# Kernel optimization log

Measured on AMD Instinct MI355X. Metric: run time of the kernel, lower is better.

## Reference

```python
import jax, jax.numpy as jnp
import numpy as np

MOS = 100        # max_output_size
IOU_T = 0.9      # iou_threshold
SCORE_T = 0.9    # score_threshold (sigma=0 -> hard NMS; also subsumes the 0.5 decode threshold)
PRE_NMS = 2048   # top-k candidates kept before greedy NMS (fixed-shape jit-friendly form)


def setup_inputs() -> dict:
    key = jax.random.key(0)
    k1, k2 = jax.random.split(key)
    B, H, W, K = 32, 192, 192, 9
    score_map = jax.random.uniform(k1, (B, H, W, K), dtype=jnp.float32)
    delta_map = jax.random.normal(k2, (B, H, W, 4 * K), dtype=jnp.float32) * 0.1
    # realistic normalized grid anchors: 3 scales x 3 aspect ratios, format (xmin, xmax, ymin, ymax)
    scales = jnp.array([0.05, 0.1, 0.2], jnp.float32)
    ratios = jnp.array([0.5, 1.0, 2.0], jnp.float32)
    ws = (scales[:, None] * jnp.sqrt(ratios)[None, :]).reshape(-1)  # [K]
    hs = (scales[:, None] / jnp.sqrt(ratios)[None, :]).reshape(-1)  # [K]
    cx = ((jnp.arange(W, dtype=jnp.float32) + 0.5) / W)[None, :, None]  # [1,W,1]
    cy = ((jnp.arange(H, dtype=jnp.float32) + 0.5) / H)[:, None, None]  # [H,1,1]
    xmin, xmax, ymin, ymax = jnp.broadcast_arrays(cx - ws / 2, cx + ws / 2, cy - hs / 2, cy + hs / 2)
    anchors = jnp.stack([xmin, xmax, ymin, ymax], axis=-1).astype(jnp.float32)  # [H,W,K,4]
    return {"score_map": score_map, "delta_map": delta_map, "anchors": anchors}


def _decode(anchors, deltas):
    # anchors: [H,W,K,4] (xmin,xmax,ymin,ymax); deltas: [B,H,W,K,4] (tx,ty,tw,th)
    xa = (anchors[..., 0] + anchors[..., 1]) * 0.5
    ya = (anchors[..., 2] + anchors[..., 3]) * 0.5
    wa = anchors[..., 1] - anchors[..., 0]
    ha = anchors[..., 3] - anchors[..., 2]
    tx, ty, tw, th = deltas[..., 0], deltas[..., 1], deltas[..., 2], deltas[..., 3]
    x = tx * wa + xa
    y = ty * ha + ya
    w = jnp.exp(tw) * wa
    h = jnp.exp(th) * ha
    # one-sided clips exactly as in the original
    xmin = jnp.maximum(x - w * 0.5, 0.0)
    xmax = jnp.minimum(x + w * 0.5, 1.0)
    ymin = jnp.maximum(y - h * 0.5, 0.0)
    ymax = jnp.minimum(y + h * 0.5, 1.0)
    # original reorders boxes for tf NMS as (ymax, xmin, ymin, xmax) and returns them in that order
    return jnp.stack([ymax, xmin, ymin, xmax], axis=-1)


def _iou_one_vs_all(box, boxes):
    # box layout: (ymax, xmin, ymin, xmax)
    y2a, x1a, y1a, x2a = box[0], box[1], box[2], box[3]
    y2b, x1b, y1b, x2b = boxes[:, 0], boxes[:, 1], boxes[:, 2], boxes[:, 3]
    area_a = jnp.maximum(y2a - y1a, 0.0) * jnp.maximum(x2a - x1a, 0.0)
    area_b = jnp.maximum(y2b - y1b, 0.0) * jnp.maximum(x2b - x1b, 0.0)
    ih = jnp.maximum(jnp.minimum(y2a, y2b) - jnp.maximum(y1a, y1b), 0.0)
    iw = jnp.maximum(jnp.minimum(x2a, x2b) - jnp.maximum(x1a, x1b), 0.0)
    inter = ih * iw
    return inter / (area_a + area_b - inter + 1e-9)


def _nms_one(scores, boxes):
    # scores: [N], boxes: [N,4]. Hard greedy NMS over top PRE_NMS candidates above SCORE_T.
    masked = jnp.where(scores > SCORE_T, scores, -jnp.inf)
    top_s, top_i = jax.lax.top_k(masked, PRE_NMS)
    top_b = boxes[top_i]  # [PRE_NMS, 4]

    def step(s, _):
        idx = jnp.argmax(s)
        valid = s[idx] > SCORE_T
        box = top_b[idx]
        iou = _iou_one_vs_all(box, top_b)
        s = jnp.where(iou > IOU_T, -jnp.inf, s).at[idx].set(-jnp.inf)
        return s, jnp.where(valid, box, jnp.zeros_like(box))

    _, out = jax.lax.scan(step, top_s, None, length=MOS)
    return out  # [MOS, 4], zero-padded past the last kept box


def reference(score_map, delta_map, anchors):
    B = score_map.shape[0]
    H, W, K = anchors.shape[:3]
    deltas = delta_map.reshape(B, H, W, K, 4)
    boxes = _decode(anchors, deltas).reshape(B, H * W * K, 4)
    scores = score_map.reshape(B, H * W * K)
    return jax.vmap(_nms_one)(scores, boxes)  # [B, MOS, 4]
```

## Files before the change

kernel.cpp:

```cpp
#include <hip/hip_runtime.h>
#include <stdint.h>

#pragma clang fp contract(off)

typedef unsigned long long u64;
typedef unsigned int u32;

#define NH 192
#define NW 192
#define NK 9
#define NPB (NH * NW * NK)
#define PRE_NMS 2048
#define CAP 4096
#define FAST_CAP 512
#define FAST_K 256
#define MOS 100
#define SCORE_T_BITS 0x3F666666u
#define SPEC_BITS   0x3F7E0000u
#define ONE_BITS 0x3F800000u
#define IOU_T 0.9f


__global__ void zero_meta(int* __restrict__ meta, int n) {
    int i = blockIdx.x * blockDim.x + threadIdx.x;
    if (i < n) meta[i] = 0;
}

__global__ void spec_compact_kernel(const uint4* __restrict__ scores,
                                    int* __restrict__ hist,
                                    int* __restrict__ cnt,
                                    u64* __restrict__ keys) {
    __shared__ u64 stage[4096];
    __shared__ int lh[256];
    __shared__ int lcount, lbase;
    const int t = threadIdx.x;
    lh[t] = 0;
    if (t == 0) lcount = 0;
    __syncthreads();
    const int b = blockIdx.y;
    const int base_i = blockIdx.x * 4096;
    const uint4* sp = scores + (size_t)b * (NPB / 4) + (size_t)blockIdx.x * 1024;
#pragma unroll
    for (int i = 0; i < 4; ++i) {
        uint4 v = sp[t + i * 256];
        int ei = base_i + (t + i * 256) * 4;
        u32 uu[4] = {v.x, v.y, v.z, v.w};
#pragma unroll
        for (int c = 0; c < 4; ++c) {
            u32 u = uu[c];
            if (u > SCORE_T_BITS) {
                atomicAdd(&lh[(u >> 16) & 0xFF], 1);
                if (u >= SPEC_BITS) {
                    int p = atomicAdd(&lcount, 1);
                    u32 idx = (u32)(ei + c);
                    stage[p] = ((u64)u << 32) | (u64)(~idx);
                }
            }
        }
    }
    __syncthreads();
    if (t == 0) lbase = atomicAdd(&cnt[b], lcount);
    if (lh[t] != 0) atomicAdd(&hist[b * 256 + t], lh[t]);
    __syncthreads();
    const int nb = lcount, gb = lbase;
    u64* kb = keys + (size_t)b * CAP;
    for (int i = t; i < nb; i += 256) {
        int gp = gb + i;
        if (gp < CAP) kb[gp] = stage[i];
    }
}

__global__ void fixup_kernel(const int* __restrict__ hist, int* __restrict__ cnt,
                             u32* __restrict__ bound, int* __restrict__ flag, int B) {
    int b = blockIdx.x * blockDim.x + threadIdx.x;
    if (b >= B) return;
    int c = cnt[b];
    if (c >= PRE_NMS && c <= CAP) { bound[b] = SPEC_BITS; flag[b] = 0; return; }
    int cum = 0, tv = 0;
    for (int v = 255; v >= 0; --v) {
        cum += hist[b * 256 + v];
        if (cum >= PRE_NMS) { tv = v; break; }
    }
    u32 bd = ((u32)(0x3F00 + tv)) << 16;
    if (bd < SCORE_T_BITS + 1) bd = SCORE_T_BITS + 1;
    bound[b] = bd; flag[b] = 1; cnt[b] = 0;
}

__global__ void repair_compact_kernel(const uint4* __restrict__ scores,
                                      const u32* __restrict__ bound,
                                      const int* __restrict__ flag,
                                      int* __restrict__ cnt,
                                      u64* __restrict__ keys) {
    const int b = blockIdx.y;
    if (!flag[b]) return;
    __shared__ u64 stage[4096];
    __shared__ int lcount, lbase;
    const int t = threadIdx.x;
    if (t == 0) lcount = 0;
    __syncthreads();
    const u32 bd = bound[b];
    const int base_i = blockIdx.x * 4096;
    const uint4* sp = scores + (size_t)b * (NPB / 4) + (size_t)blockIdx.x * 1024;
#pragma unroll
    for (int i = 0; i < 4; ++i) {
        uint4 v = sp[t + i * 256];
        int ei = base_i + (t + i * 256) * 4;
        u32 uu[4] = {v.x, v.y, v.z, v.w};
#pragma unroll
        for (int c = 0; c < 4; ++c) {
            if (uu[c] >= bd) {
                int p = atomicAdd(&lcount, 1);
                u32 idx = (u32)(ei + c);
                stage[p] = ((u64)uu[c] << 32) | (u64)(~idx);
            }
        }
    }
    __syncthreads();
    if (t == 0) lbase = atomicAdd(&cnt[b], lcount);
    __syncthreads();
    const int nb = lcount, gb = lbase;
    u64* kb = keys + (size_t)b * CAP;
    for (int i = t; i < nb; i += 256) {
        int gp = gb + i;
        if (gp < CAP) kb[gp] = stage[i];
    }
}

__device__ __forceinline__ float4 decode_box(u64 key, int b,
                                             const float4* __restrict__ anchors4,
                                             const float4* __restrict__ deltas4) {
    u32 idx = ~(u32)(key & 0xFFFFFFFFu);
    float4 a = anchors4[idx];
    float4 d = deltas4[(size_t)b * NPB + idx];
    float xa = (a.x + a.y) * 0.5f;
    float ya = (a.z + a.w) * 0.5f;
    float wa = a.y - a.x;
    float ha = a.w - a.z;
    float x = d.x * wa + xa;
    float y = d.y * ha + ya;
    float w = expf(d.z) * wa;
    float h = expf(d.w) * ha;
    float4 bx;
    bx.x = fminf(y + h * 0.5f, 1.f);
    bx.y = fmaxf(x - w * 0.5f, 0.f);
    bx.z = fmaxf(y - h * 0.5f, 0.f);
    bx.w = fminf(x + w * 0.5f, 1.f);
    return bx;
}

__device__ __forceinline__ int wave_nms(const float4* __restrict__ boxes, int n,
                                        float4* __restrict__ out4, int lane) {
    float4 pb0 = make_float4(0.f, 0.f, 0.f, 0.f), pb1 = pb0;
    float pa0 = 0.f, pa1 = 0.f;
    int np = 0;
#define ACCEPT(cb, ar) do { \
        if (lane == (np & 63)) { \
            if (np < 64) { pb0 = cb; pa0 = ar; } else { pb1 = cb; pa1 = ar; } \
            out4[np] = cb; } \
        ++np; } while (0)
    for (int j = 0; j < n; j += 2) {
        const bool have1 = (j + 1 < n);
        float4 c0 = boxes[j];
        float4 c1 = boxes[have1 ? j + 1 : j];
        float ar0 = fmaxf(c0.x - c0.z, 0.f) * fmaxf(c0.w - c0.y, 0.f);
        float ar1 = fmaxf(c1.x - c1.z, 0.f) * fmaxf(c1.w - c1.y, 0.f);
        bool s0 = false, s1 = false;
        if (lane < np) {
            float ih = fmaxf(fminf(pb0.x, c0.x) - fmaxf(pb0.z, c0.z), 0.f);
            float iw = fmaxf(fminf(pb0.w, c0.w) - fmaxf(pb0.y, c0.y), 0.f);
            float inter = ih * iw;
            s0 = inter / (pa0 + ar0 - inter + 1e-9f) > IOU_T;
            ih = fmaxf(fminf(pb0.x, c1.x) - fmaxf(pb0.z, c1.z), 0.f);
            iw = fmaxf(fminf(pb0.w, c1.w) - fmaxf(pb0.y, c1.y), 0.f);
            inter = ih * iw;
            s1 = inter / (pa0 + ar1 - inter + 1e-9f) > IOU_T;
        }
        if (lane + 64 < np) {
            float ih = fmaxf(fminf(pb1.x, c0.x) - fmaxf(pb1.z, c0.z), 0.f);
            float iw = fmaxf(fminf(pb1.w, c0.w) - fmaxf(pb1.y, c0.y), 0.f);
            float inter = ih * iw;
            s0 = s0 || (inter / (pa1 + ar0 - inter + 1e-9f) > IOU_T);
            ih = fmaxf(fminf(pb1.x, c1.x) - fmaxf(pb1.z, c1.z), 0.f);
            iw = fmaxf(fminf(pb1.w, c1.w) - fmaxf(pb1.y, c1.y), 0.f);
            inter = ih * iw;
            s1 = s1 || (inter / (pa1 + ar1 - inter + 1e-9f) > IOU_T);
        }
        bool acc0 = !__any(s0);
        bool acc1 = !__any(s1);
        if (acc0) {
            ACCEPT(c0, ar0);
            if (np == MOS) break;
            if (have1 && acc1) {
                float ih = fmaxf(fminf(c0.x, c1.x) - fmaxf(c0.z, c1.z), 0.f);
                float iw = fmaxf(fminf(c0.w, c1.w) - fmaxf(c0.y, c1.y), 0.f);
                float inter = ih * iw;
                if (!(inter / (ar0 + ar1 - inter + 1e-9f) > IOU_T)) {
                    ACCEPT(c1, ar1);
                    if (np == MOS) break;
                }
            }
        } else if (have1 && acc1) {
            ACCEPT(c1, ar1);
            if (np == MOS) break;
        }
    }
#undef ACCEPT
    return np;
}

__global__ __launch_bounds__(256) void sort_nms_kernel(
        const float* __restrict__ deltas, const float* __restrict__ anchors,
        const int* __restrict__ cnt, const u32* __restrict__ bound,
        const u64* __restrict__ keys, float* __restrict__ out) {
    __shared__ __align__(16) u64 key_s[CAP];
    __shared__ __align__(16) float4 boxes[PRE_NMS];
    __shared__ u64 fast_k[FAST_CAP];
    __shared__ int lh[256];
    __shared__ int s_cnt, s_nsel, s_flag, s_cbin, s_sh;

    const int t = threadIdx.x;
    const int b = blockIdx.x;
    const int nc = min(cnt[b], CAP);
    const u64* kb = keys + (size_t)b * CAP;
    const float4* anchors4 = (const float4*)anchors;
    const float4* deltas4  = (const float4*)deltas;
    float4* out4 = (float4*)out + (size_t)b * MOS;

    lh[t] = 0;
    if (t == 0) {
        s_cnt = 0;
        u32 dmax = ONE_BITS - bound[b];
        int bits = 32 - __builtin_clz(dmax);
        s_sh = (bits > 8) ? (bits - 8) : 0;
    }
    __syncthreads();
    const int sh = s_sh;

#pragma unroll
    for (int p = 0; p < CAP / 256; ++p) {
        int i = t + p * 256;
        u64 k = (i < nc) ? kb[i] : 0ULL;
        key_s[i] = k;
        if (i < nc) {
            u32 d = ONE_BITS - (u32)(k >> 32);
            u32 bin = d >> sh;
            if (bin > 255u) bin = 255u;
            atomicAdd(&lh[bin], 1);
        }
    }
    for (int i = t; i < FAST_CAP; i += 256) fast_k[i] = 0ULL;
    __syncthreads();

    if (t == 0) {
        int cum = 0; bool hit = false;
        for (int v = 0; v < 256; ++v) {
            cum += lh[v];
            if (cum >= FAST_K) {
                if (cum > FAST_CAP) { s_nsel = cum - lh[v]; s_cbin = v - 1; }
                else                { s_nsel = cum;         s_cbin = v; }
                hit = true; break;
            }
        }
        if (!hit) { s_nsel = cum; s_cbin = 255; }
    }
    __syncthreads();
    const int cbin = s_cbin;
    const int n_sel = s_nsel;

#pragma unroll
    for (int p = 0; p < CAP / 256; ++p) {
        int i = t + p * 256;
        if (i < nc) {
            u64 k = key_s[i];
            u32 d = ONE_BITS - (u32)(k >> 32);
            u32 bin = d >> sh;
            if (bin > 255u) bin = 255u;
            if ((int)bin <= cbin) fast_k[atomicAdd(&s_cnt, 1)] = k;
        }
    }
    __syncthreads();

    for (int k = 2; k <= FAST_CAP; k <<= 1) {
        for (int j = k >> 1; j > 0; j >>= 1) {
            for (int i = t; i < FAST_CAP; i += 256) {
                int ix = i ^ j;
                if (ix > i) {
                    u64 a = fast_k[i], c = fast_k[ix];
                    bool up = ((i & k) == 0);
                    if (up ? (a < c) : (a > c)) { fast_k[i] = c; fast_k[ix] = a; }
                }
            }
            __syncthreads();
        }
    }

    for (int i = t; i < FAST_CAP; i += 256)
        boxes[i] = (i < n_sel) ? decode_box(fast_k[i], b, anchors4, deltas4)
                               : make_float4(0.f, 0.f, 0.f, 0.f);
    __syncthreads();

    if (t < 64) {
        int np = wave_nms(boxes, n_sel, out4, t);
        bool success = (np == MOS) || (n_sel == nc);
        if (success)
            for (int i = np + t; i < MOS; i += 64)
                out4[i] = make_float4(0.f, 0.f, 0.f, 0.f);
        if (t == 0) s_flag = success ? 1 : 0;
    }
    __syncthreads();
    if (s_flag) return;

    for (int k = 2; k <= CAP; k <<= 1) {
        for (int j = k >> 1; j > 0; j >>= 1) {
            for (int i = t; i < CAP; i += 256) {
                int ix = i ^ j;
                if (ix > i) {
                    u64 a = key_s[i], c = key_s[ix];
                    bool up = ((i & k) == 0);
                    if (up ? (a < c) : (a > c)) { key_s[i] = c; key_s[ix] = a; }
                }
            }
            __syncthreads();
        }
    }
    const int nvalid = min(nc, PRE_NMS);
    for (int i = t; i < PRE_NMS; i += 256)
        boxes[i] = (i < nvalid) ? decode_box(key_s[i], b, anchors4, deltas4)
                                : make_float4(0.f, 0.f, 0.f, 0.f);
    __syncthreads();
    if (t < 64) {
        int np = wave_nms(boxes, nvalid, out4, t);
        for (int i = np + t; i < MOS; i += 64)
            out4[i] = make_float4(0.f, 0.f, 0.f, 0.f);
    }
}

extern "C" void kernel_launch(void* const* d_in, const int* in_sizes, int n_in,
                              void* d_out, int out_size, void* d_ws, size_t ws_size,
                              hipStream_t stream) {
    const float* score_map = (const float*)d_in[0];
    const float* delta_map = (const float*)d_in[1];
    const float* anchors   = (const float*)d_in[2];
    float* out = (float*)d_out;
    const int B = in_sizes[0] / NPB;

    char* ws = (char*)d_ws;
    size_t off = 0;
    int* hist  = (int*)(ws + off); off += (size_t)B * 256 * 4;
    int* cnt   = (int*)(ws + off); off += (size_t)B * 4;
    u32* bound = (u32*)(ws + off); off += (size_t)B * 4;
    int* flag  = (int*)(ws + off); off += (size_t)B * 4;
    u64* keys  = (u64*)(ws + off);

    const int meta_n = B * 256 + B;
    zero_meta<<<(meta_n + 255) / 256, 256, 0, stream>>>(hist, meta_n);
    spec_compact_kernel<<<dim3(NPB / 4096, B), 256, 0, stream>>>(
        (const uint4*)score_map, hist, cnt, keys);
    fixup_kernel<<<1, 64, 0, stream>>>(hist, cnt, bound, flag, B);
    repair_compact_kernel<<<dim3(NPB / 4096, B), 256, 0, stream>>>(
        (const uint4*)score_map, bound, flag, cnt, keys);
    sort_nms_kernel<<<B, 256, 0, stream>>>(delta_map, anchors, cnt, bound, keys, out);
}
```

Baseline: 301.0 us.

## Drop histogram and repair launches, move fallback selection into sort kernel

The speculative compaction kernel no longer builds a per-batch histogram and uses a smaller staging buffer. The separate fixup and repair kernels are removed. A batch whose speculative count falls outside the valid range now rescans its scores inside the sort/NMS block, using a two-level histogram to pick a finer bound. The NMS loop also prefetches the next pair of candidate boxes from shared memory. This cuts two kernel launches and the histogram atomics on the common path, but the rare fallback path becomes a serial per-block scan of a whole image.

```diff
diff --git a/kernel.cpp b/kernel.cpp
--- a/kernel.cpp
+++ b/kernel.cpp
@@ -21,20 +21,17 @@
 #define IOU_T 0.9f
 
 
-__global__ void zero_meta(int* __restrict__ meta, int n) {
-    int i = blockIdx.x * blockDim.x + threadIdx.x;
-    if (i < n) meta[i] = 0;
+__global__ void zero_cnt(int* __restrict__ cnt, int n) {
+    int i = threadIdx.x;
+    if (i < n) cnt[i] = 0;
 }
 
 __global__ void spec_compact_kernel(const uint4* __restrict__ scores,
-                                    int* __restrict__ hist,
                                     int* __restrict__ cnt,
                                     u64* __restrict__ keys) {
-    __shared__ u64 stage[4096];
-    __shared__ int lh[256];
+    __shared__ u64 stage[512];
     __shared__ int lcount, lbase;
     const int t = threadIdx.x;
-    lh[t] = 0;
     if (t == 0) lcount = 0;
     __syncthreads();
     const int b = blockIdx.y;
@@ -48,77 +45,17 @@
 #pragma unroll
         for (int c = 0; c < 4; ++c) {
             u32 u = uu[c];
-            if (u > SCORE_T_BITS) {
-                atomicAdd(&lh[(u >> 16) & 0xFF], 1);
-                if (u >= SPEC_BITS) {
-                    int p = atomicAdd(&lcount, 1);
-                    u32 idx = (u32)(ei + c);
-                    stage[p] = ((u64)u << 32) | (u64)(~idx);
-                }
-            }
-        }
-    }
-    __syncthreads();
-    if (t == 0) lbase = atomicAdd(&cnt[b], lcount);
-    if (lh[t] != 0) atomicAdd(&hist[b * 256 + t], lh[t]);
-    __syncthreads();
-    const int nb = lcount, gb = lbase;
-    u64* kb = keys + (size_t)b * CAP;
-    for (int i = t; i < nb; i += 256) {
-        int gp = gb + i;
-        if (gp < CAP) kb[gp] = stage[i];
-    }
-}
-
-__global__ void fixup_kernel(const int* __restrict__ hist, int* __restrict__ cnt,
-                             u32* __restrict__ bound, int* __restrict__ flag, int B) {
-    int b = blockIdx.x * blockDim.x + threadIdx.x;
-    if (b >= B) return;
-    int c = cnt[b];
-    if (c >= PRE_NMS && c <= CAP) { bound[b] = SPEC_BITS; flag[b] = 0; return; }
-    int cum = 0, tv = 0;
-    for (int v = 255; v >= 0; --v) {
-        cum += hist[b * 256 + v];
-        if (cum >= PRE_NMS) { tv = v; break; }
-    }
-    u32 bd = ((u32)(0x3F00 + tv)) << 16;
-    if (bd < SCORE_T_BITS + 1) bd = SCORE_T_BITS + 1;
-    bound[b] = bd; flag[b] = 1; cnt[b] = 0;
-}
-
-__global__ void repair_compact_kernel(const uint4* __restrict__ scores,
-                                      const u32* __restrict__ bound,
-                                      const int* __restrict__ flag,
-                                      int* __restrict__ cnt,
-                                      u64* __restrict__ keys) {
-    const int b = blockIdx.y;
-    if (!flag[b]) return;
-    __shared__ u64 stage[4096];
-    __shared__ int lcount, lbase;
-    const int t = threadIdx.x;
-    if (t == 0) lcount = 0;
-    __syncthreads();
-    const u32 bd = bound[b];
-    const int base_i = blockIdx.x * 4096;
-    const uint4* sp = scores + (size_t)b * (NPB / 4) + (size_t)blockIdx.x * 1024;
-#pragma unroll
-    for (int i = 0; i < 4; ++i) {
-        uint4 v = sp[t + i * 256];
-        int ei = base_i + (t + i * 256) * 4;
-        u32 uu[4] = {v.x, v.y, v.z, v.w};
-#pragma unroll
-        for (int c = 0; c < 4; ++c) {
-            if (uu[c] >= bd) {
+            if (u >= SPEC_BITS) {
                 int p = atomicAdd(&lcount, 1);
                 u32 idx = (u32)(ei + c);
-                stage[p] = ((u64)uu[c] << 32) | (u64)(~idx);
+                if (p < 512) stage[p] = ((u64)u << 32) | (u64)(~idx);
             }
         }
     }
     __syncthreads();
     if (t == 0) lbase = atomicAdd(&cnt[b], lcount);
     __syncthreads();
-    const int nb = lcount, gb = lbase;
+    const int nb = min(lcount, 512), gb = lbase;
     u64* kb = keys + (size_t)b * CAP;
     for (int i = t; i < nb; i += 256) {
         int gp = gb + i;
@@ -153,15 +90,21 @@
     float4 pb0 = make_float4(0.f, 0.f, 0.f, 0.f), pb1 = pb0;
     float pa0 = 0.f, pa1 = 0.f;
     int np = 0;
+    if (n <= 0) return 0;
 #define ACCEPT(cb, ar) do { \
         if (lane == (np & 63)) { \
             if (np < 64) { pb0 = cb; pa0 = ar; } else { pb1 = cb; pa1 = ar; } \
             out4[np] = cb; } \
         ++np; } while (0)
+    float4 n0 = boxes[0];
+    float4 n1 = boxes[(1 < n) ? 1 : 0];
     for (int j = 0; j < n; j += 2) {
         const bool have1 = (j + 1 < n);
-        float4 c0 = boxes[j];
-        float4 c1 = boxes[have1 ? j + 1 : j];
+        float4 c0 = n0, c1 = n1;
+        int jn0 = (j + 2 < n) ? j + 2 : j;
+        int jn1 = (j + 3 < n) ? j + 3 : jn0;
+        n0 = boxes[jn0];
+        n1 = boxes[jn1];
         float ar0 = fmaxf(c0.x - c0.z, 0.f) * fmaxf(c0.w - c0.y, 0.f);
         float ar1 = fmaxf(c1.x - c1.z, 0.f) * fmaxf(c1.w - c1.y, 0.f);
         bool s0 = false, s1 = false;
@@ -209,40 +152,128 @@
 }
 
 __global__ __launch_bounds__(256) void sort_nms_kernel(
+        const uint4* __restrict__ scores,
         const float* __restrict__ deltas, const float* __restrict__ anchors,
-        const int* __restrict__ cnt, const u32* __restrict__ bound,
-        const u64* __restrict__ keys, float* __restrict__ out) {
+        const int* __restrict__ cnt, const u64* __restrict__ keys,
+        float* __restrict__ out) {
     __shared__ __align__(16) u64 key_s[CAP];
     __shared__ __align__(16) float4 boxes[PRE_NMS];
     __shared__ u64 fast_k[FAST_CAP];
     __shared__ int lh[256];
-    __shared__ int s_cnt, s_nsel, s_flag, s_cbin, s_sh;
+    __shared__ int s_cnt, s_nsel, s_flag, s_cbin, s_sh, s_nc;
+    __shared__ u32 s_bd;
+    __shared__ int s_tv, s_cumabove, s_skipB;
 
     const int t = threadIdx.x;
     const int b = blockIdx.x;
-    const int nc = min(cnt[b], CAP);
-    const u64* kb = keys + (size_t)b * CAP;
     const float4* anchors4 = (const float4*)anchors;
     const float4* deltas4  = (const float4*)deltas;
     float4* out4 = (float4*)out + (size_t)b * MOS;
 
-    lh[t] = 0;
+    const int nc0 = cnt[b];
+    const bool valid = (nc0 >= PRE_NMS && nc0 <= CAP);
+
+    if (valid) {
+        const u64* kb = keys + (size_t)b * CAP;
+#pragma unroll
+        for (int p = 0; p < CAP / 256; ++p) {
+            int i = t + p * 256;
+            key_s[i] = (i < nc0) ? kb[i] : 0ULL;
+        }
+        if (t == 0) { s_nc = nc0; s_bd = SPEC_BITS; }
+        __syncthreads();
+    } else {
+        const uint4* sp = scores + (size_t)b * (NPB / 4);
+        lh[t] = 0;
+        __syncthreads();
+        for (int i = t; i < NPB / 4; i += 256) {
+            uint4 v = sp[i];
+            u32 uu[4] = {v.x, v.y, v.z, v.w};
+#pragma unroll
+            for (int c = 0; c < 4; ++c)
+                if (uu[c] > SCORE_T_BITS) atomicAdd(&lh[(uu[c] >> 16) & 0xFF], 1);
+        }
+        __syncthreads();
+        if (t == 0) {
+            int cum = 0, tv = -1, cumab = 0;
+            for (int v = 255; v >= 0; --v) {
+                int h = lh[v];
+                if (cum + h >= PRE_NMS) { tv = v; cumab = cum; break; }
+                cum += h;
+            }
+            if (tv < 0) { s_bd = SCORE_T_BITS + 1; s_skipB = 1; }
+            else        { s_tv = tv; s_cumabove = cumab; s_skipB = 0; }
+        }
+        __syncthreads();
+        if (!s_skipB) {
+            const int tv = s_tv;
+            lh[t] = 0;
+            __syncthreads();
+            for (int i = t; i < NPB / 4; i += 256) {
+                uint4 v = sp[i];
+                u32 uu[4] = {v.x, v.y, v.z, v.w};
+#pragma unroll
+                for (int c = 0; c < 4; ++c)
+                    if (uu[c] > SCORE_T_BITS && (int)((uu[c] >> 16) & 0xFF) == tv)
+                        atomicAdd(&lh[(uu[c] >> 8) & 0xFF], 1);
+            }
+            __syncthreads();
+            if (t == 0) {
+                int cum = s_cumabove, iv = 0;
+                for (int v = 255; v >= 0; --v) {
+                    cum += lh[v];
+                    if (cum >= PRE_NMS) {
+                        iv = (cum > CAP && v < 255) ? v + 1 : v;
+                        break;
+                    }
+                }
+                u32 bd = (((u32)(0x3F00 + tv)) << 16) | ((u32)iv << 8);
+                if (bd < SCORE_T_BITS + 1) bd = SCORE_T_BITS + 1;
+                s_bd = bd;
+            }
+        }
+        __syncthreads();
+        if (t == 0) s_cnt = 0;
+        __syncthreads();
+        const u32 bd = s_bd;
+        for (int i = t; i < NPB / 4; i += 256) {
+            uint4 v = sp[i];
+            u32 uu[4] = {v.x, v.y, v.z, v.w};
+#pragma unroll
+            for (int c = 0; c < 4; ++c) {
+                if (uu[c] >= bd) {
+                    int p = atomicAdd(&s_cnt, 1);
+                    u32 idx = (u32)(i * 4 + c);
+                    if (p < CAP) key_s[p] = ((u64)uu[c] << 32) | (u64)(~idx);
+                }
+            }
+        }
+        __syncthreads();
+        if (t == 0) s_nc = min(s_cnt, CAP);
+        __syncthreads();
+        for (int p = 0; p < CAP / 256; ++p) {
+            int i = t + p * 256;
+            if (i >= s_nc) key_s[i] = 0ULL;
+        }
+        __syncthreads();
+    }
+
+    const int nc = s_nc;
     if (t == 0) {
         s_cnt = 0;
-        u32 dmax = ONE_BITS - bound[b];
+        u32 dmax = ONE_BITS - s_bd;
         int bits = 32 - __builtin_clz(dmax);
         s_sh = (bits > 8) ? (bits - 8) : 0;
     }
+    lh[t] = 0;
     __syncthreads();
     const int sh = s_sh;
 
 #pragma unroll
     for (int p = 0; p < CAP / 256; ++p) {
         int i = t + p * 256;
-        u64 k = (i < nc) ? kb[i] : 0ULL;
-        key_s[i] = k;
         if (i < nc) {
-            u32 d = ONE_BITS - (u32)(k >> 32);
+            u32 d = ONE_BITS - (u32)(key_s[i] >> 32);
             u32 bin = d >> sh;
             if (bin > 255u) bin = 255u;
             atomicAdd(&lh[bin], 1);
@@ -345,19 +376,13 @@
     const int B = in_sizes[0] / NPB;
 
     char* ws = (char*)d_ws;
-    size_t off = 0;
-    int* hist  = (int*)(ws + off); off += (size_t)B * 256 * 4;
-    int* cnt   = (int*)(ws + off); off += (size_t)B * 4;
-    u32* bound = (u32*)(ws + off); off += (size_t)B * 4;
-    int* flag  = (int*)(ws + off); off += (size_t)B * 4;
-    u64* keys  = (u64*)(ws + off);
-
-    const int meta_n = B * 256 + B;
-    zero_meta<<<(meta_n + 255) / 256, 256, 0, stream>>>(hist, meta_n);
+    int* cnt  = (int*)ws;
+    u64* keys = (u64*)(ws + (size_t)B * 4 + 4);
+    keys = (u64*)(((uintptr_t)keys + 15) & ~(uintptr_t)15);
+
+    zero_cnt<<<1, 64, 0, stream>>>(cnt, B);
     spec_compact_kernel<<<dim3(NPB / 4096, B), 256, 0, stream>>>(
-        (const uint4*)score_map, hist, cnt, keys);
-    fixup_kernel<<<1, 64, 0, stream>>>(hist, cnt, bound, flag, B);
-    repair_compact_kernel<<<dim3(NPB / 4096, B), 256, 0, stream>>>(
-        (const uint4*)score_map, bound, flag, cnt, keys);
-    sort_nms_kernel<<<B, 256, 0, stream>>>(delta_map, anchors, cnt, bound, keys, out);
-}
+        (const uint4*)score_map, cnt, keys);
+    sort_nms_kernel<<<B, 256, 0, stream>>>(
+        (const uint4*)score_map, delta_map, anchors, cnt, keys, out);
+}
```

Result: no change. 297.6 us (-1.1%).
